# Kernel tuning notes

Measured on AMD Instinct MI355X. Metric: run time of the kernel, lower is better.

## Reference

```python
import jax, jax.numpy as jnp
import numpy as np

DIM = 3
SIGMA_MIN = 0.05
NORM_EPS = 1e-10
DEG2RAD = np.pi / 180.0


def setup_inputs() -> dict:
    key = jax.random.key(0)
    kF, = jax.random.split(key, 1)
    B = 4_000_000
    F = jax.random.normal(kF, (B, 3, 3), dtype=jnp.float32)
    return {
        "F": F,
        "youngs_modulus_log": jnp.asarray(np.log(2_000_000.0), dtype=jnp.float32),
        "poissons_ratio": jnp.asarray(0.4, dtype=jnp.float32),
        "friction_angle": jnp.asarray(25.0, dtype=jnp.float32),
        "cohesion": jnp.asarray(0.0, dtype=jnp.float32),
    }


def reference(F, youngs_modulus_log, poissons_ratio, friction_angle, cohesion):
    E = jnp.exp(youngs_modulus_log)
    sin_phi = jnp.sin(friction_angle * DEG2RAD)
    alpha = jnp.sqrt(2.0 / 3.0) * 2.0 * sin_phi / (3.0 - sin_phi)
    mu = E / (2.0 * (1.0 + poissons_ratio))
    la = E * poissons_ratio / ((1.0 + poissons_ratio) * (1.0 - 2.0 * poissons_ratio))

    # Batched 3x3 SVD: U (B,3,3), sigma (B,3), Vh (B,3,3)
    U, sigma, Vh = jnp.linalg.svd(F, full_matrices=False)

    sigma = jnp.maximum(sigma, SIGMA_MIN)
    eps = jnp.log(sigma)                                   # log strain (B,3)
    trace = eps.sum(axis=1, keepdims=True)                 # (B,1)
    eps_hat = eps - trace / DIM                            # deviatoric part
    eps_hat_norm = jnp.maximum(
        jnp.linalg.norm(eps_hat, axis=1, keepdims=True), NORM_EPS)
    shifted_trace = trace - cohesion * DIM
    cond_yield = shifted_trace < 0.0                       # (B,1)
    delta_gamma = eps_hat_norm + (DIM * la + 2.0 * mu) / (2.0 * mu) * shifted_trace * alpha
    compress_eps = eps - jnp.maximum(delta_gamma, 0.0) / eps_hat_norm * eps_hat
    expand_eps = jnp.ones_like(eps) * cohesion
    eps_corrected = jnp.where(cond_yield, compress_eps, expand_eps)

    # F_corrected = U @ diag(exp(eps_corrected)) @ Vh
    F_corrected = jnp.einsum('bij,bj,bjk->bik', U, jnp.exp(eps_corrected), Vh)
    return F_corrected
```

## Files before the change

### kernel.cpp

```cpp
#include <hip/hip_runtime.h>
#include <math.h>

#define BLOCK 256

__device__ __forceinline__ float frcp(float x) { return __builtin_amdgcn_rcpf(x); }
__device__ __forceinline__ float frsq(float x) { return __builtin_amdgcn_rsqf(x); }

__device__ __forceinline__ void jacobi_cs(float app, float apq, float aqq,
                                          float& c, float& s, float& t) {
    float tau = (aqq - app) * 0.5f * frcp(apq);
    float tt  = copysignf(1.0f, tau) * frcp(fabsf(tau) + sqrtf(fmaf(tau, tau, 1.0f)));
    bool z = (apq == 0.0f);
    t = z ? 0.0f : tt;
    c = frsq(fmaf(t, t, 1.0f));
    s = t * c;
}

__device__ __forceinline__ void qr_givens(float x, float y, float& c, float& s) {
    float d = fmaf(x, x, y * y);
    bool ok = d > 1e-30f;
    float inv = frsq(fmaxf(d, 1e-30f));
    c = ok ? x * inv : 1.0f;
    s = ok ? y * inv : 0.0f;
}

__global__ __launch_bounds__(BLOCK) void dp_kernel(
    const float* __restrict__ F,
    const float* __restrict__ p_yml,
    const float* __restrict__ p_nu,
    const float* __restrict__ p_fa,
    const float* __restrict__ p_coh,
    float* __restrict__ out,
    int n_elem)
{
    __shared__ float lds[BLOCK * 9];
    const int t_id = threadIdx.x;
    const long long base_f = (long long)blockIdx.x * (BLOCK * 9);
    const long long nfloats = (long long)n_elem * 9LL;

    #pragma unroll
    for (int j = 0; j < 3; ++j) {
        int idx = t_id + j * BLOCK;
        if (idx < (BLOCK * 9) / 4) {
            long long g4 = base_f / 4 + idx;
            long long gf = g4 * 4;
            if (gf + 3 < nfloats) {
                ((float4*)lds)[idx] = ((const float4*)F)[g4];
            } else {
                #pragma unroll
                for (int k = 0; k < 4; ++k)
                    if (gf + k < nfloats) lds[idx * 4 + k] = F[gf + k];
            }
        }
    }
    __syncthreads();

    const long long e = (long long)blockIdx.x * BLOCK + t_id;
    const bool valid = e < n_elem;

    float a00, a01, a02, a10, a11, a12, a20, a21, a22;
    {
        const float* p = lds + t_id * 9;
        a00 = p[0]; a01 = p[1]; a02 = p[2];
        a10 = p[3]; a11 = p[4]; a12 = p[5];
        a20 = p[6]; a21 = p[7]; a22 = p[8];
    }
    __syncthreads();

    const float yml = p_yml[0];
    const float nu  = p_nu[0];
    const float fa  = p_fa[0];
    const float coh = p_coh[0];
    const float E     = expf(yml);
    const float sphi  = sinf(fa * 0.017453292519943295f);
    const float alpha = 0.816496580927726f * 2.0f * sphi / (3.0f - sphi);
    const float mu    = E / (2.0f * (1.0f + nu));
    const float la    = E * nu / ((1.0f + nu) * (1.0f - 2.0f * nu));
    const float ratio = (3.0f * la + 2.0f * mu) / (2.0f * mu) * alpha;

    float s00 = a00*a00 + a10*a10 + a20*a20;
    float s01 = a00*a01 + a10*a11 + a20*a21;
    float s02 = a00*a02 + a10*a12 + a20*a22;
    float s11 = a01*a01 + a11*a11 + a21*a21;
    float s12 = a01*a02 + a11*a12 + a21*a22;
    float s22 = a02*a02 + a12*a12 + a22*a22;

    float v00=1.f,v01=0.f,v02=0.f, v10=0.f,v11=1.f,v12=0.f, v20=0.f,v21=0.f,v22=1.f;
    float c, s, tj, t0, t1;
    #pragma unroll
    for (int sweep = 0; sweep < 4; ++sweep) {
        jacobi_cs(s00, s01, s11, c, s, tj);
        s00 = s00 - tj * s01;  s11 = s11 + tj * s01;  s01 = 0.0f;
        t0 = s02; t1 = s12;  s02 = c*t0 - s*t1;  s12 = s*t0 + c*t1;
        t0=v00; t1=v01; v00=c*t0-s*t1; v01=s*t0+c*t1;
        t0=v10; t1=v11; v10=c*t0-s*t1; v11=s*t0+c*t1;
        t0=v20; t1=v21; v20=c*t0-s*t1; v21=s*t0+c*t1;
        jacobi_cs(s00, s02, s22, c, s, tj);
        s00 = s00 - tj * s02;  s22 = s22 + tj * s02;  s02 = 0.0f;
        t0 = s01; t1 = s12;  s01 = c*t0 - s*t1;  s12 = s*t0 + c*t1;
        t0=v00; t1=v02; v00=c*t0-s*t1; v02=s*t0+c*t1;
        t0=v10; t1=v12; v10=c*t0-s*t1; v12=s*t0+c*t1;
        t0=v20; t1=v22; v20=c*t0-s*t1; v22=s*t0+c*t1;
        jacobi_cs(s11, s12, s22, c, s, tj);
        s11 = s11 - tj * s12;  s22 = s22 + tj * s12;  s12 = 0.0f;
        t0 = s01; t1 = s02;  s01 = c*t0 - s*t1;  s02 = s*t0 + c*t1;
        t0=v01; t1=v02; v01=c*t0-s*t1; v02=s*t0+c*t1;
        t0=v11; t1=v12; v11=c*t0-s*t1; v12=s*t0+c*t1;
        t0=v21; t1=v22; v21=c*t0-s*t1; v22=s*t0+c*t1;
    }

    {
        float tmp; bool sw;
        sw = s00 < s11;
        if (sw) { tmp=s00;s00=s11;s11=tmp; tmp=v00;v00=v01;v01=tmp;
                  tmp=v10;v10=v11;v11=tmp; tmp=v20;v20=v21;v21=tmp; }
        sw = s00 < s22;
        if (sw) { tmp=s00;s00=s22;s22=tmp; tmp=v00;v00=v02;v02=tmp;
                  tmp=v10;v10=v12;v12=tmp; tmp=v20;v20=v22;v22=tmp; }
        sw = s11 < s22;
        if (sw) { tmp=s11;s11=s22;s22=tmp; tmp=v01;v01=v02;v02=tmp;
                  tmp=v11;v11=v12;v12=tmp; tmp=v21;v21=v22;v22=tmp; }
    }

    float b00 = a00*v00 + a01*v10 + a02*v20;
    float b01 = a00*v01 + a01*v11 + a02*v21;
    float b02 = a00*v02 + a01*v12 + a02*v22;
    float b10 = a10*v00 + a11*v10 + a12*v20;
    float b11 = a10*v01 + a11*v11 + a12*v21;
    float b12 = a10*v02 + a11*v12 + a12*v22;
    float b20 = a20*v00 + a21*v10 + a22*v20;
    float b21 = a20*v01 + a21*v11 + a22*v21;
    float b22 = a20*v02 + a21*v12 + a22*v22;

    float u00=1.f,u01=0.f,u02=0.f, u10=0.f,u11=1.f,u12=0.f, u20=0.f,u21=0.f,u22=1.f;

    qr_givens(b00, b10, c, s);
    t0=b00; b00=c*t0+s*b10;
    t0=b01; b01=c*t0+s*b11; b11=c*b11-s*t0;
    t0=b02; b02=c*t0+s*b12; b12=c*b12-s*t0;
    t0=u00; u00=c*t0+s*u01; u01=c*u01-s*t0;
    t0=u10; u10=c*t0+s*u11; u11=c*u11-s*t0;
    t0=u20; u20=c*t0+s*u21; u21=c*u21-s*t0;

    qr_givens(b00, b20, c, s);
    t0=b00; b00=c*t0+s*b20;
    t0=b01; b01=c*t0+s*b21; b21=c*b21-s*t0;
    t0=b02; b02=c*t0+s*b22; b22=c*b22-s*t0;
    t0=u00; u00=c*t0+s*u02; u02=c*u02-s*t0;
    t0=u10; u10=c*t0+s*u12; u12=c*u12-s*t0;
    t0=u20; u20=c*t0+s*u22; u22=c*u22-s*t0;

    qr_givens(b11, b21, c, s);
    t0=b11; b11=c*t0+s*b21;
    t0=b12; b12=c*t0+s*b22; b22=c*b22-s*t0;
    t0=u01; u01=c*t0+s*u02; u02=c*u02-s*t0;
    t0=u11; u11=c*t0+s*u12; u12=c*u12-s*t0;
    t0=u21; u21=c*t0+s*u22; u22=c*u22-s*t0;

    float sgn = b22 < 0.0f ? -1.0f : 1.0f;
    float sg2 = b22 * sgn;
    u02 *= sgn; u12 *= sgn; u22 *= sgn;

    float sig0 = fmaxf(b00, 0.05f);
    float sig1 = fmaxf(b11, 0.05f);
    float sig2 = fmaxf(sg2, 0.05f);
    float e0 = logf(sig0), e1 = logf(sig1), e2 = logf(sig2);
    float tr  = e0 + e1 + e2;
    float tr3 = tr * (1.0f / 3.0f);
    float h0 = e0 - tr3, h1 = e1 - tr3, h2 = e2 - tr3;
    float hn = sqrtf(h0*h0 + h1*h1 + h2*h2);
    hn = fmaxf(hn, 1e-10f);
    float st = tr - coh * 3.0f;
    float dg = hn + ratio * st;
    float sc = fmaxf(dg, 0.0f) * frcp(hn);
    bool yield = st < 0.0f;
    float ec0 = yield ? (e0 - sc * h0) : coh;
    float ec1 = yield ? (e1 - sc * h1) : coh;
    float ec2 = yield ? (e2 - sc * h2) : coh;
    float f0 = expf(ec0), f1 = expf(ec1), f2 = expf(ec2);

    float w00=u00*f0, w01=u01*f1, w02=u02*f2;
    float w10=u10*f0, w11=u11*f1, w12=u12*f2;
    float w20=u20*f0, w21=u21*f1, w22=u22*f2;
    float r00 = w00*v00 + w01*v01 + w02*v02;
    float r01 = w00*v10 + w01*v11 + w02*v12;
    float r02 = w00*v20 + w01*v21 + w02*v22;
    float r10 = w10*v00 + w11*v01 + w12*v02;
    float r11 = w10*v10 + w11*v11 + w12*v12;
    float r12 = w10*v20 + w11*v21 + w12*v22;
    float r20 = w20*v00 + w21*v01 + w22*v02;
    float r21 = w20*v10 + w21*v11 + w22*v12;
    float r22 = w20*v20 + w21*v21 + w22*v22;

    if (valid) {
        float* p = lds + t_id * 9;
        p[0]=r00; p[1]=r01; p[2]=r02;
        p[3]=r10; p[4]=r11; p[5]=r12;
        p[6]=r20; p[7]=r21; p[8]=r22;
    }
    __syncthreads();

    #pragma unroll
    for (int j = 0; j < 3; ++j) {
        int idx = t_id + j * BLOCK;
        if (idx < (BLOCK * 9) / 4) {
            long long g4 = base_f / 4 + idx;
            long long gf = g4 * 4;
            if (gf + 3 < nfloats) {
                ((float4*)out)[g4] = ((float4*)lds)[idx];
            } else {
                #pragma unroll
                for (int k = 0; k < 4; ++k)
                    if (gf + k < nfloats) out[gf + k] = lds[idx * 4 + k];
            }
        }
    }
}

extern "C" void kernel_launch(void* const* d_in, const int* in_sizes, int n_in,
                              void* d_out, int out_size, void* d_ws, size_t ws_size,
                              hipStream_t stream) {
    const float* F = (const float*)d_in[0];
    const int n_elem = in_sizes[0] / 9;
    const int grid = (n_elem + BLOCK - 1) / BLOCK;
    dp_kernel<<<grid, BLOCK, 0, stream>>>(
        F,
        (const float*)d_in[1], (const float*)d_in[2],
        (const float*)d_in[3], (const float*)d_in[4],
        (float*)d_out, n_elem);
}
```

Before: 288.7 us.

## Replace two-sided Jacobi plus QR with one-sided Jacobi SVD and fast intrinsics

Replaces the Gram-matrix eigen-Jacobi, sort and Givens QR with a one-sided Jacobi that orthogonalises the columns of F directly. Each rotation also swaps columns so singular values come out ordered. U's first two columns come from normalised columns, the third from a cross product, and the determinant sign is folded into the last exponent. Fast intrinsics (__expf, __logf, rcp) replace the accurate math calls. The goal is fewer ALU ops per element and shorter dependency chains, at the risk of accuracy loss on ill-conditioned or rank-deficient matrices, since each rotation recomputes three column dot products.

```diff
diff --git a/kernel.cpp b/kernel.cpp
--- a/kernel.cpp
+++ b/kernel.cpp
@@ -6,22 +6,35 @@
 __device__ __forceinline__ float frcp(float x) { return __builtin_amdgcn_rcpf(x); }
 __device__ __forceinline__ float frsq(float x) { return __builtin_amdgcn_rsqf(x); }
 
-__device__ __forceinline__ void jacobi_cs(float app, float apq, float aqq,
-                                          float& c, float& s, float& t) {
-    float tau = (aqq - app) * 0.5f * frcp(apq);
-    float tt  = copysignf(1.0f, tau) * frcp(fabsf(tau) + sqrtf(fmaf(tau, tau, 1.0f)));
-    bool z = (apq == 0.0f);
-    t = z ? 0.0f : tt;
-    c = frsq(fmaf(t, t, 1.0f));
-    s = t * c;
-}
-
-__device__ __forceinline__ void qr_givens(float x, float y, float& c, float& s) {
-    float d = fmaf(x, x, y * y);
-    bool ok = d > 1e-30f;
-    float inv = frsq(fmaxf(d, 1e-30f));
-    c = ok ? x * inv : 1.0f;
-    s = ok ? y * inv : 0.0f;
+__device__ __forceinline__ void onesided_rot(
+    float& x0, float& x1, float& x2,
+    float& y0, float& y1, float& y2,
+    float& p0, float& p1, float& p2,
+    float& q0, float& q1, float& q2)
+{
+    float app = fmaf(x0, x0, fmaf(x1, x1, x2 * x2));
+    float aqq = fmaf(y0, y0, fmaf(y1, y1, y2 * y2));
+    float apq = fmaf(x0, y0, fmaf(x1, y1, x2 * y2));
+    float del = app - aqq;
+    float rho = apq + apq;
+    float r   = sqrtf(fmaf(del, del, rho * rho));
+    float ch = fabsf(del) + r;
+    float sh = (del < 0.0f) ? -rho : rho;
+    float n2 = fmaf(ch, ch, sh * sh);
+    float inv = frsq(n2);
+    bool ok = n2 > 1e-30f;
+    float c = ok ? ch * inv : 1.0f;
+    float s = ok ? sh * inv : 0.0f;
+    bool sw = del < 0.0f;
+    float cf = sw ? -s : c;
+    float sf = sw ?  c : s;
+    float t;
+    t = x0; x0 = fmaf(cf, t, sf * y0); y0 = fmaf(cf, y0, -sf * t);
+    t = x1; x1 = fmaf(cf, t, sf * y1); y1 = fmaf(cf, y1, -sf * t);
+    t = x2; x2 = fmaf(cf, t, sf * y2); y2 = fmaf(cf, y2, -sf * t);
+    t = p0; p0 = fmaf(cf, t, sf * q0); q0 = fmaf(cf, q0, -sf * t);
+    t = p1; p1 = fmaf(cf, t, sf * q1); q1 = fmaf(cf, q1, -sf * t);
+    t = p2; p2 = fmaf(cf, t, sf * q2); q2 = fmaf(cf, q2, -sf * t);
 }
 
 __global__ __launch_bounds__(BLOCK) void dp_kernel(
@@ -71,126 +84,66 @@
     const float nu  = p_nu[0];
     const float fa  = p_fa[0];
     const float coh = p_coh[0];
-    const float E     = expf(yml);
-    const float sphi  = sinf(fa * 0.017453292519943295f);
-    const float alpha = 0.816496580927726f * 2.0f * sphi / (3.0f - sphi);
-    const float mu    = E / (2.0f * (1.0f + nu));
-    const float la    = E * nu / ((1.0f + nu) * (1.0f - 2.0f * nu));
-    const float ratio = (3.0f * la + 2.0f * mu) / (2.0f * mu) * alpha;
-
-    float s00 = a00*a00 + a10*a10 + a20*a20;
-    float s01 = a00*a01 + a10*a11 + a20*a21;
-    float s02 = a00*a02 + a10*a12 + a20*a22;
-    float s11 = a01*a01 + a11*a11 + a21*a21;
-    float s12 = a01*a02 + a11*a12 + a21*a22;
-    float s22 = a02*a02 + a12*a12 + a22*a22;
+    const float E     = __expf(yml);
+    const float sphi  = __sinf(fa * 0.017453292519943295f);
+    const float alpha = 1.632993161855452f * sphi * frcp(3.0f - sphi);
+    const float mu    = E * 0.5f * frcp(1.0f + nu);
+    const float la    = E * nu * frcp((1.0f + nu) * (1.0f - 2.0f * nu));
+    const float ratio = (3.0f * la + 2.0f * mu) * frcp(2.0f * mu) * alpha;
 
     float v00=1.f,v01=0.f,v02=0.f, v10=0.f,v11=1.f,v12=0.f, v20=0.f,v21=0.f,v22=1.f;
-    float c, s, tj, t0, t1;
     #pragma unroll
     for (int sweep = 0; sweep < 4; ++sweep) {
-        jacobi_cs(s00, s01, s11, c, s, tj);
-        s00 = s00 - tj * s01;  s11 = s11 + tj * s01;  s01 = 0.0f;
-        t0 = s02; t1 = s12;  s02 = c*t0 - s*t1;  s12 = s*t0 + c*t1;
-        t0=v00; t1=v01; v00=c*t0-s*t1; v01=s*t0+c*t1;
-        t0=v10; t1=v11; v10=c*t0-s*t1; v11=s*t0+c*t1;
-        t0=v20; t1=v21; v20=c*t0-s*t1; v21=s*t0+c*t1;
-        jacobi_cs(s00, s02, s22, c, s, tj);
-        s00 = s00 - tj * s02;  s22 = s22 + tj * s02;  s02 = 0.0f;
-        t0 = s01; t1 = s12;  s01 = c*t0 - s*t1;  s12 = s*t0 + c*t1;
-        t0=v00; t1=v02; v00=c*t0-s*t1; v02=s*t0+c*t1;
-        t0=v10; t1=v12; v10=c*t0-s*t1; v12=s*t0+c*t1;
-        t0=v20; t1=v22; v20=c*t0-s*t1; v22=s*t0+c*t1;
-        jacobi_cs(s11, s12, s22, c, s, tj);
-        s11 = s11 - tj * s12;  s22 = s22 + tj * s12;  s12 = 0.0f;
-        t0 = s01; t1 = s02;  s01 = c*t0 - s*t1;  s02 = s*t0 + c*t1;
-        t0=v01; t1=v02; v01=c*t0-s*t1; v02=s*t0+c*t1;
-        t0=v11; t1=v12; v11=c*t0-s*t1; v12=s*t0+c*t1;
-        t0=v21; t1=v22; v21=c*t0-s*t1; v22=s*t0+c*t1;
+        onesided_rot(a00,a10,a20, a01,a11,a21, v00,v10,v20, v01,v11,v21);
+        onesided_rot(a00,a10,a20, a02,a12,a22, v00,v10,v20, v02,v12,v22);
+        onesided_rot(a01,a11,a21, a02,a12,a22, v01,v11,v21, v02,v12,v22);
     }
 
-    {
-        float tmp; bool sw;
-        sw = s00 < s11;
-        if (sw) { tmp=s00;s00=s11;s11=tmp; tmp=v00;v00=v01;v01=tmp;
-                  tmp=v10;v10=v11;v11=tmp; tmp=v20;v20=v21;v21=tmp; }
-        sw = s00 < s22;
-        if (sw) { tmp=s00;s00=s22;s22=tmp; tmp=v00;v00=v02;v02=tmp;
-                  tmp=v10;v10=v12;v12=tmp; tmp=v20;v20=v22;v22=tmp; }
-        sw = s11 < s22;
-        if (sw) { tmp=s11;s11=s22;s22=tmp; tmp=v01;v01=v02;v02=tmp;
-                  tmp=v11;v11=v12;v12=tmp; tmp=v21;v21=v22;v22=tmp; }
-    }
+    float n0sq = fmaf(a00,a00, fmaf(a10,a10, a20*a20));
+    float n1sq = fmaf(a01,a01, fmaf(a11,a11, a21*a21));
+    float i0 = frsq(fmaxf(n0sq, 1e-30f));
+    float i1 = frsq(fmaxf(n1sq, 1e-30f));
+    float u00 = a00*i0, u10 = a10*i0, u20 = a20*i0;
+    float u01 = a01*i1, u11 = a11*i1, u21 = a21*i1;
+    float sig0 = n0sq * i0;
+    float sig1 = n1sq * i1;
+    float u02 = fmaf(u10, u21, -u20*u11);
+    float u12 = fmaf(u20, u01, -u00*u21);
+    float u22 = fmaf(u00, u11, -u10*u01);
+    float d3  = fmaf(u02, a02, fmaf(u12, a12, u22*a22));
+    float sig2 = fabsf(d3);
 
-    float b00 = a00*v00 + a01*v10 + a02*v20;
-    float b01 = a00*v01 + a01*v11 + a02*v21;
-    float b02 = a00*v02 + a01*v12 + a02*v22;
-    float b10 = a10*v00 + a11*v10 + a12*v20;
-    float b11 = a10*v01 + a11*v11 + a12*v21;
-    float b12 = a10*v02 + a11*v12 + a12*v22;
-    float b20 = a20*v00 + a21*v10 + a22*v20;
-    float b21 = a20*v01 + a21*v11 + a22*v21;
-    float b22 = a20*v02 + a21*v12 + a22*v22;
-
-    float u00=1.f,u01=0.f,u02=0.f, u10=0.f,u11=1.f,u12=0.f, u20=0.f,u21=0.f,u22=1.f;
-
-    qr_givens(b00, b10, c, s);
-    t0=b00; b00=c*t0+s*b10;
-    t0=b01; b01=c*t0+s*b11; b11=c*b11-s*t0;
-    t0=b02; b02=c*t0+s*b12; b12=c*b12-s*t0;
-    t0=u00; u00=c*t0+s*u01; u01=c*u01-s*t0;
-    t0=u10; u10=c*t0+s*u11; u11=c*u11-s*t0;
-    t0=u20; u20=c*t0+s*u21; u21=c*u21-s*t0;
-
-    qr_givens(b00, b20, c, s);
-    t0=b00; b00=c*t0+s*b20;
-    t0=b01; b01=c*t0+s*b21; b21=c*b21-s*t0;
-    t0=b02; b02=c*t0+s*b22; b22=c*b22-s*t0;
-    t0=u00; u00=c*t0+s*u02; u02=c*u02-s*t0;
-    t0=u10; u10=c*t0+s*u12; u12=c*u12-s*t0;
-    t0=u20; u20=c*t0+s*u22; u22=c*u22-s*t0;
-
-    qr_givens(b11, b21, c, s);
-    t0=b11; b11=c*t0+s*b21;
-    t0=b12; b12=c*t0+s*b22; b22=c*b22-s*t0;
-    t0=u01; u01=c*t0+s*u02; u02=c*u02-s*t0;
-    t0=u11; u11=c*t0+s*u12; u12=c*u12-s*t0;
-    t0=u21; u21=c*t0+s*u22; u22=c*u22-s*t0;
-
-    float sgn = b22 < 0.0f ? -1.0f : 1.0f;
-    float sg2 = b22 * sgn;
-    u02 *= sgn; u12 *= sgn; u22 *= sgn;
-
-    float sig0 = fmaxf(b00, 0.05f);
-    float sig1 = fmaxf(b11, 0.05f);
-    float sig2 = fmaxf(sg2, 0.05f);
-    float e0 = logf(sig0), e1 = logf(sig1), e2 = logf(sig2);
+    float e0 = __logf(fmaxf(sig0, 0.05f));
+    float e1 = __logf(fmaxf(sig1, 0.05f));
+    float e2 = __logf(fmaxf(sig2, 0.05f));
     float tr  = e0 + e1 + e2;
     float tr3 = tr * (1.0f / 3.0f);
     float h0 = e0 - tr3, h1 = e1 - tr3, h2 = e2 - tr3;
-    float hn = sqrtf(h0*h0 + h1*h1 + h2*h2);
+    float hn = sqrtf(fmaf(h0,h0, fmaf(h1,h1, h2*h2)));
     hn = fmaxf(hn, 1e-10f);
     float st = tr - coh * 3.0f;
     float dg = hn + ratio * st;
     float sc = fmaxf(dg, 0.0f) * frcp(hn);
     bool yield = st < 0.0f;
-    float ec0 = yield ? (e0 - sc * h0) : coh;
-    float ec1 = yield ? (e1 - sc * h1) : coh;
-    float ec2 = yield ? (e2 - sc * h2) : coh;
-    float f0 = expf(ec0), f1 = expf(ec1), f2 = expf(ec2);
+    float ec0 = yield ? fmaf(-sc, h0, e0) : coh;
+    float ec1 = yield ? fmaf(-sc, h1, e1) : coh;
+    float ec2 = yield ? fmaf(-sc, h2, e2) : coh;
+    float f0 = __expf(ec0);
+    float f1 = __expf(ec1);
+    float f2 = copysignf(__expf(ec2), d3);
 
-    float w00=u00*f0, w01=u01*f1, w02=u02*f2;
-    float w10=u10*f0, w11=u11*f1, w12=u12*f2;
-    float w20=u20*f0, w21=u21*f1, w22=u22*f2;
-    float r00 = w00*v00 + w01*v01 + w02*v02;
-    float r01 = w00*v10 + w01*v11 + w02*v12;
-    float r02 = w00*v20 + w01*v21 + w02*v22;
-    float r10 = w10*v00 + w11*v01 + w12*v02;
-    float r11 = w10*v10 + w11*v11 + w12*v12;
-    float r12 = w10*v20 + w11*v21 + w12*v22;
-    float r20 = w20*v00 + w21*v01 + w22*v02;
-    float r21 = w20*v10 + w21*v11 + w22*v12;
-    float r22 = w20*v20 + w21*v21 + w22*v22;
+    float w00 = u00*f0, w01 = u01*f1, w02 = u02*f2;
+    float w10 = u10*f0, w11 = u11*f1, w12 = u12*f2;
+    float w20 = u20*f0, w21 = u21*f1, w22 = u22*f2;
+    float r00 = fmaf(w00,v00, fmaf(w01,v01, w02*v02));
+    float r01 = fmaf(w00,v10, fmaf(w01,v11, w02*v12));
+    float r02 = fmaf(w00,v20, fmaf(w01,v21, w02*v22));
+    float r10 = fmaf(w10,v00, fmaf(w11,v01, w12*v02));
+    float r11 = fmaf(w10,v10, fmaf(w11,v11, w12*v12));
+    float r12 = fmaf(w10,v20, fmaf(w11,v21, w12*v22));
+    float r20 = fmaf(w20,v00, fmaf(w21,v01, w22*v02));
+    float r21 = fmaf(w20,v10, fmaf(w21,v11, w22*v12));
+    float r22 = fmaf(w20,v20, fmaf(w21,v21, w22*v22));
 
     if (valid) {
         float* p = lds + t_id * 9;
```

Result: faster. 275.0 us (-4.8%).
